# Performance work log

Hardware: AMD Instinct MI355X
Metric: run time of the kernel (lower is better)

Reference implementation:

```python
import jax, jax.numpy as jnp
import numpy as np

EMBED = 128
HEADS = 8
HEAD_DIM = EMBED // HEADS


def setup_inputs() -> dict:
    key = jax.random.key(0)
    ks = jax.random.split(key, 11)
    B, T, N, C = 8, 64, 170, EMBED
    s = 1.0 / np.sqrt(C)
    return {
        "values": jax.random.normal(ks[0], (B, T, N, C), dtype=jnp.float32),
        "keys": jax.random.normal(ks[1], (B, T, N, C), dtype=jnp.float32),
        "query": jax.random.normal(ks[2], (B, T, N, C), dtype=jnp.float32),
        "Wv": jax.random.normal(ks[3], (C, C), dtype=jnp.float32) * s,
        "bv": jnp.zeros((C,), dtype=jnp.float32),
        "Wk": jax.random.normal(ks[4], (C, C), dtype=jnp.float32) * s,
        "bk": jnp.zeros((C,), dtype=jnp.float32),
        "Wq": jax.random.normal(ks[5], (C, C), dtype=jnp.float32) * s,
        "bq": jnp.zeros((C,), dtype=jnp.float32),
        "Wo": jax.random.normal(ks[6], (C, C), dtype=jnp.float32) * s,
        "bo": jnp.zeros((C,), dtype=jnp.float32),
    }


def reference(values, keys, query, Wv, bv, Wk, bk, Wq, bq, Wo, bo):
    B, T, N, C = query.shape
    H, D = HEADS, HEAD_DIM
    # Linear projections (torch nn.Linear: x @ W.T + b)
    v = (values @ Wv.T + bv).reshape(B, T, N, H, D)
    k = (keys @ Wk.T + bk).reshape(B, T, N, H, D)
    q = (query @ Wq.T + bq).reshape(B, T, N, H, D)
    # spatial mode: attention over nodes N, independent per (b, t, h)
    energy = jnp.einsum('btqhd,btkhd->btqkh', q, k)  # [B,T,N,N,H]
    scale = jnp.asarray(C, q.dtype) ** 0.5
    attn = jax.nn.softmax(energy / scale, axis=3)
    out = jnp.einsum('btqkh,btkhd->btqhd', attn, v).reshape(B, T, N, H * D)
    return out @ Wo.T + bo
```

## Files before the change

kernel.cpp:

```cpp
#include <hip/hip_runtime.h>
#include <cstdint>

typedef float   f32x4  __attribute__((ext_vector_type(4)));
typedef __bf16  bf16x4 __attribute__((ext_vector_type(4)));
typedef __bf16  bf16x8 __attribute__((ext_vector_type(8)));

#if __has_builtin(__builtin_amdgcn_exp2f)
#define EXP2F(x) __builtin_amdgcn_exp2f(x)
#else
#define EXP2F(x) exp2f(x)
#endif

#define BT_TOTAL 512
#define NNODES 170
#define CDIM 128
#define HEADS 8
#define HDIM 16
#define SLAB (NNODES*HDIM)
#define NPAD 176
#define VSLAB (HDIM*NPAD)
#define QKV_ELEMS ((size_t)BT_TOTAL*HEADS*SLAB)
#define WPAD 136
#define S2L2E 0.12753851f

__global__ __launch_bounds__(256) void wconv_kernel(const float* __restrict__ wq,
                                                    const float* __restrict__ wk,
                                                    const float* __restrict__ wv,
                                                    const float* __restrict__ wo,
                                                    __bf16* __restrict__ wbf) {
    int idx = blockIdx.x * 256 + threadIdx.x;
    if (idx >= 4 * 16384) return;
    int mat = idx >> 14, rem = idx & 16383;
    int c = rem >> 7, o = rem & 127;
    int kk = o >> 5, l4 = (o & 31) >> 3, j = o & 7;
    int col = kk * 32 + l4 * 4 + (j & 3) + 16 * (j >> 2);
    const float* W = (mat == 0) ? wq : (mat == 1) ? wk : (mat == 2) ? wv : wo;
    float scale = (mat == 0) ? S2L2E : 1.0f;
    wbf[idx] = (__bf16)(W[c * 128 + col] * scale);
}

__global__ __launch_bounds__(256, 4) void qkv_kernel(const float* __restrict__ qin,
    const float* __restrict__ kin, const float* __restrict__ vin,
    const __bf16* __restrict__ wbf,
    const float* __restrict__ bq, const float* __restrict__ bk, const float* __restrict__ bv,
    __bf16* __restrict__ qws, __bf16* __restrict__ kws, __bf16* __restrict__ vt) {
    __shared__ __bf16 Wl[128 * WPAD];
    int t = threadIdx.x;
    int iid = blockIdx.x / BT_TOTAL;
    int bt  = blockIdx.x % BT_TOTAL;
    const float* X    = (iid == 0) ? qin : (iid == 1) ? kin : vin;
    const float* bias = (iid == 0) ? bq  : (iid == 1) ? bk  : bv;
    float wscale = (iid == 0) ? S2L2E : 1.0f;
    const __bf16* wb = wbf + iid * 16384;
    #pragma unroll
    for (int i = 0; i < 8; ++i) {
        int idx = i * 256 + t;
        int c = idx >> 4, x = (idx & 15) * 8;
        *(bf16x8*)&Wl[c * WPAD + x] = *(const bf16x8*)&wb[idx * 8];
    }
    __syncthreads();

    int w = t >> 6, lane = t & 63, li = lane & 15, l4 = lane >> 4;
    const f32x4 zf = {0.f, 0.f, 0.f, 0.f};

    auto loadA = [&](f32x4* A, int tile) {
        int mrow = tile * 16 + li;
        bool v = mrow < NNODES;
        const float* xr = X + ((size_t)(bt * NNODES + mrow)) * CDIM;
        #pragma unroll
        for (int kk = 0; kk < 4; ++kk) {
            A[2 * kk]     = v ? *(const f32x4*)(xr + kk * 32 + l4 * 4)      : zf;
            A[2 * kk + 1] = v ? *(const f32x4*)(xr + kk * 32 + l4 * 4 + 16) : zf;
        }
    };
    auto compute = [&](const f32x4* A, int tile) {
        f32x4 acc[8] = {};
        #pragma unroll
        for (int kk = 0; kk < 4; ++kk) {
            f32x4 a0 = A[2 * kk], a1 = A[2 * kk + 1];
            bf16x8 a = { (__bf16)a0[0], (__bf16)a0[1], (__bf16)a0[2], (__bf16)a0[3],
                         (__bf16)a1[0], (__bf16)a1[1], (__bf16)a1[2], (__bf16)a1[3] };
            #pragma unroll
            for (int nt = 0; nt < 8; ++nt) {
                bf16x8 b = *(const bf16x8*)&Wl[(nt * 16 + li) * WPAD + kk * 32 + l4 * 8];
                if (iid < 2)
                    acc[nt] = __builtin_amdgcn_mfma_f32_16x16x32_bf16(b, a, acc[nt], 0, 0, 0);
                else
                    acc[nt] = __builtin_amdgcn_mfma_f32_16x16x32_bf16(a, b, acc[nt], 0, 0, 0);
            }
        }
        if (iid < 2) {
            __bf16* dst = ((iid == 0) ? qws : kws) + (size_t)bt * HEADS * SLAB;
            int n = tile * 16 + li;
            if (n < NNODES) {
                #pragma unroll
                for (int nt = 0; nt < 8; ++nt) {
                    f32x4 b4 = *(const f32x4*)&bias[nt * 16 + l4 * 4];
                    f32x4 ov = acc[nt] + b4 * wscale;
                    bf16x4 o4 = { (__bf16)ov[0], (__bf16)ov[1], (__bf16)ov[2], (__bf16)ov[3] };
                    *(bf16x4*)&dst[(size_t)nt * SLAB + n * HDIM + l4 * 4] = o4;
                }
            }
        } else {
            __bf16* dst = vt + (size_t)bt * HEADS * VSLAB;
            int n0 = tile * 16 + l4 * 4;
            #pragma unroll
            for (int nt = 0; nt < 8; ++nt) {
                float bval = bias[nt * 16 + li];
                __bf16* d2 = dst + (size_t)nt * VSLAB + li * NPAD + n0;
                if (n0 + 3 < NNODES) {
                    bf16x4 o4 = { (__bf16)(acc[nt][0] + bval), (__bf16)(acc[nt][1] + bval),
                                  (__bf16)(acc[nt][2] + bval), (__bf16)(acc[nt][3] + bval) };
                    *(bf16x4*)d2 = o4;
                } else {
                    #pragma unroll
                    for (int r = 0; r < 4; ++r)
                        if (n0 + r < NNODES) d2[r] = (__bf16)(acc[nt][r] + bval);
                }
            }
        }
    };

    f32x4 A0[8], A1[8];
    loadA(A0, w);
    loadA(A1, w + 4);
    compute(A0, w);
    if (w < 3) loadA(A0, w + 8);
    compute(A1, w + 4);
    if (w < 3) compute(A0, w + 8);
}

__global__ __launch_bounds__(256) void attn_kernel(const __bf16* __restrict__ qws,
                                                   const __bf16* __restrict__ kws,
                                                   const __bf16* __restrict__ vt,
                                                   __bf16* __restrict__ ows) {
    int unit = blockIdx.x * 4 + (threadIdx.x >> 6);
    int half = unit & 1, bh = unit >> 1;
    int bt = bh >> 3, h = bh & 7;
    int lane = threadIdx.x & 63, li = lane & 15, l4 = lane >> 4;
    const __bf16* qb  = qws + ((size_t)(bt * HEADS + h)) * SLAB;
    const __bf16* kb  = kws + ((size_t)(bt * HEADS + h)) * SLAB;
    const __bf16* vtb = vt  + ((size_t)(bt * HEADS + h)) * VSLAB;
    __bf16* ob = ows + (size_t)bt * NNODES * CDIM + (h >> 1) * 32 + (h & 1) * 4;
    const __bf16 bz = (__bf16)0.0f;
    const bf16x4 z4 = {bz, bz, bz, bz};
    const f32x4 zf = {0.f, 0.f, 0.f, 0.f};

    bf16x4 kf[11];
    #pragma unroll
    for (int tt = 0; tt < 11; ++tt)
        kf[tt] = *(const bf16x4*)&kb[(tt * 16 + li) * HDIM + l4 * 4];

    bf16x8 vf[6];
    #pragma unroll
    for (int s = 0; s < 5; ++s) {
        bf16x4 a = *(const bf16x4*)&vtb[li * NPAD + 32 * s + 4 * l4];
        bf16x4 b = *(const bf16x4*)&vtb[li * NPAD + 32 * s + 4 * l4 + 16];
        vf[s] = __builtin_shufflevector(a, b, 0, 1, 2, 3, 4, 5, 6, 7);
    }
    {
        bf16x4 a = *(const bf16x4*)&vtb[li * NPAD + 160 + 4 * l4];
        bf16x8 v5 = { (160 + 4 * l4 + 0 < NNODES) ? a[0] : bz,
                      (160 + 4 * l4 + 1 < NNODES) ? a[1] : bz,
                      (160 + 4 * l4 + 2 < NNODES) ? a[2] : bz,
                      (160 + 4 * l4 + 3 < NNODES) ? a[3] : bz,
                      bz, bz, bz, bz };
        vf[5] = v5;
    }

    int q0 = half ? 6 : 0;
    int qn = half ? 5 : 6;
    for (int qi = 0; qi < qn; ++qi) {
        int qc = q0 + qi;
        bf16x4 qv = *(const bf16x4*)&qb[(qc * 16 + li) * HDIM + l4 * 4];
        bf16x8 qf = __builtin_shufflevector(qv, z4, 0, 1, 2, 3, 4, 5, 6, 7);
        bf16x4 ph[11];
        f32x4 s4 = zf;
        #pragma unroll
        for (int tt = 0; tt < 11; ++tt) {
            bf16x8 a = __builtin_shufflevector(kf[tt], z4, 0, 1, 2, 3, 4, 5, 6, 7);
            f32x4 e = __builtin_amdgcn_mfma_f32_16x16x32_bf16(a, qf, zf, 0, 0, 0);
            if (tt == 10) {
                #pragma unroll
                for (int r = 0; r < 4; ++r)
                    e[r] = (160 + l4 * 4 + r < NNODES) ? e[r] : -1.0e30f;
            }
            f32x4 p;
            p[0] = EXP2F(e[0]); p[1] = EXP2F(e[1]);
            p[2] = EXP2F(e[2]); p[3] = EXP2F(e[3]);
            s4 += p;
            ph[tt] = __builtin_convertvector(p, bf16x4);
        }
        float sum = (s4[0] + s4[1]) + (s4[2] + s4[3]);
        sum += __shfl_xor(sum, 16);
        sum += __shfl_xor(sum, 32);
        float inv = 1.0f / sum;
        f32x4 o0 = zf, o1 = zf;
        o0 = __builtin_amdgcn_mfma_f32_16x16x32_bf16(vf[0],
                __builtin_shufflevector(ph[0], ph[1], 0,1,2,3,4,5,6,7), o0, 0,0,0);
        o1 = __builtin_amdgcn_mfma_f32_16x16x32_bf16(vf[1],
                __builtin_shufflevector(ph[2], ph[3], 0,1,2,3,4,5,6,7), o1, 0,0,0);
        o0 = __builtin_amdgcn_mfma_f32_16x16x32_bf16(vf[2],
                __builtin_shufflevector(ph[4], ph[5], 0,1,2,3,4,5,6,7), o0, 0,0,0);
        o1 = __builtin_amdgcn_mfma_f32_16x16x32_bf16(vf[3],
                __builtin_shufflevector(ph[6], ph[7], 0,1,2,3,4,5,6,7), o1, 0,0,0);
        o0 = __builtin_amdgcn_mfma_f32_16x16x32_bf16(vf[4],
                __builtin_shufflevector(ph[8], ph[9], 0,1,2,3,4,5,6,7), o0, 0,0,0);
        o1 = __builtin_amdgcn_mfma_f32_16x16x32_bf16(vf[5],
                __builtin_shufflevector(ph[10], z4,    0,1,2,3,4,5,6,7), o1, 0,0,0);
        f32x4 o = (o0 + o1) * inv;
        int q = qc * 16 + li;
        if (q < NNODES) {
            bf16x4 ov = { (__bf16)o[0], (__bf16)o[1], (__bf16)o[2], (__bf16)o[3] };
            *(bf16x4*)&ob[(size_t)q * CDIM + l4 * 8] = ov;
        }
    }
}

__global__ __launch_bounds__(512) void oproj_kernel(const __bf16* __restrict__ ows,
                                                    const __bf16* __restrict__ wbf,
                                                    const float* __restrict__ bo,
                                                    float* __restrict__ out) {
    __shared__ __bf16 Wl[128 * WPAD];
    int t = threadIdx.x;
    int bt = blockIdx.x;
    const __bf16* wo = wbf + 3 * 16384;
    #pragma unroll
    for (int i = 0; i < 4; ++i) {
        int idx = i * 512 + t;
        int c = idx >> 4, x = (idx & 15) * 8;
        *(bf16x8*)&Wl[c * WPAD + x] = *(const bf16x8*)&wo[idx * 8];
    }
    __syncthreads();

    int w = t >> 6, lane = t & 63, li = lane & 15, l4 = lane >> 4;
    const bf16x8 z8 = {};

    auto loadO = [&](bf16x8* A, int tile) {
        int mrow = tile * 16 + li;
        bool v = mrow < NNODES;
        const __bf16* ar = ows + ((size_t)(bt * NNODES + mrow)) * CDIM;
        #pragma unroll
        for (int kk = 0; kk < 4; ++kk)
            A[kk] = v ? *(const bf16x8*)(ar + kk * 32 + l4 * 8) : z8;
    };
    auto computeO = [&](const bf16x8* A, int tile) {
        f32x4 acc[8] = {};
        #pragma unroll
        for (int kk = 0; kk < 4; ++kk) {
            #pragma unroll
            for (int nt = 0; nt < 8; ++nt) {
                bf16x8 b = *(const bf16x8*)&Wl[(nt * 16 + li) * WPAD + kk * 32 + l4 * 8];
                acc[nt] = __builtin_amdgcn_mfma_f32_16x16x32_bf16(b, A[kk], acc[nt], 0, 0, 0);
            }
        }
        int n = tile * 16 + li;
        if (n < NNODES) {
            float* orow = out + ((size_t)bt * NNODES + n) * CDIM;
            #pragma unroll
            for (int nt = 0; nt < 8; ++nt) {
                f32x4 b4 = *(const f32x4*)&bo[nt * 16 + l4 * 4];
                *(f32x4*)&orow[nt * 16 + l4 * 4] = acc[nt] + b4;
            }
        }
    };

    bf16x8 A0[4], A1[4];
    loadO(A0, w);
    if (w < 3) loadO(A1, w + 8);
    computeO(A0, w);
    if (w < 3) computeO(A1, w + 8);
}

extern "C" void kernel_launch(void* const* d_in, const int* in_sizes, int n_in,
                              void* d_out, int out_size, void* d_ws, size_t ws_size,
                              hipStream_t stream) {
    const float* values = (const float*)d_in[0];
    const float* keys   = (const float*)d_in[1];
    const float* query  = (const float*)d_in[2];
    const float* Wv = (const float*)d_in[3];
    const float* bv = (const float*)d_in[4];
    const float* Wk = (const float*)d_in[5];
    const float* bk = (const float*)d_in[6];
    const float* Wq = (const float*)d_in[7];
    const float* bq = (const float*)d_in[8];
    const float* Wo = (const float*)d_in[9];
    const float* bo = (const float*)d_in[10];
    float* out = (float*)d_out;

    __bf16* qws = (__bf16*)d_ws;
    __bf16* kws = qws + QKV_ELEMS;
    __bf16* ows = kws + QKV_ELEMS;
    __bf16* wbf = ows + QKV_ELEMS;
    __bf16* vt  = (__bf16*)d_out;

    hipLaunchKernelGGL(wconv_kernel, dim3(256),  dim3(256), 0, stream, Wq, Wk, Wv, Wo, wbf);
    hipLaunchKernelGGL(qkv_kernel,   dim3(1536), dim3(256), 0, stream,
                       query, keys, values, wbf, bq, bk, bv, qws, kws, vt);
    hipLaunchKernelGGL(attn_kernel,  dim3(2048), dim3(256), 0, stream, qws, kws, vt, ows);
    hipLaunchKernelGGL(oproj_kernel, dim3(512),  dim3(512), 0, stream, ows, wbf, bo, out);
}
```

Before: 103.5 us.

## Restructure QKV projection over flat rows with async global-to-LDS staging

The QKV projection kernel now tiles the flattened B*T*N row space in 64-row blocks instead of one (b,t) slab per block, which removes the padding waste of 170-node slabs. Input rows are staged into a double-buffered LDS tile using global_load_lds with a swizzled layout to avoid bank conflicts. Each wave keeps its half of the weight matrix in registers rather than in a shared LDS weight tile. The trade-offs are more blocks, per-row div/mod by 170 in the epilogue, and higher register pressure from holding weight fragments.

Result: slower. 113.5 us (+9.7%).

```diff
diff --git a/kernel.cpp b/kernel.cpp
--- a/kernel.cpp
+++ b/kernel.cpp
@@ -22,6 +22,13 @@
 #define QKV_ELEMS ((size_t)BT_TOTAL*HEADS*SLAB)
 #define WPAD 136
 #define S2L2E 0.12753851f
+#define MROWS (BT_TOTAL*NNODES)
+#define BLKS_PER_IID 1360
+
+__device__ __forceinline__ void gload_lds16(const float* g, float* l) {
+    __builtin_amdgcn_global_load_lds((const __attribute__((address_space(1))) uint32_t*)g,
+                                     (__attribute__((address_space(3))) uint32_t*)l, 16, 0, 0);
+}
 
 __global__ __launch_bounds__(256) void wconv_kernel(const float* __restrict__ wq,
                                                     const float* __restrict__ wk,
@@ -44,90 +51,102 @@
     const __bf16* __restrict__ wbf,
     const float* __restrict__ bq, const float* __restrict__ bk, const float* __restrict__ bv,
     __bf16* __restrict__ qws, __bf16* __restrict__ kws, __bf16* __restrict__ vt) {
-    __shared__ __bf16 Wl[128 * WPAD];
-    int t = threadIdx.x;
-    int iid = blockIdx.x / BT_TOTAL;
-    int bt  = blockIdx.x % BT_TOTAL;
+    __shared__ __align__(16) float Xl[2][32 * 128];
+
+    int bid = blockIdx.x;
+    int iid = bid / BLKS_PER_IID, blk = bid % BLKS_PER_IID;
     const float* X    = (iid == 0) ? qin : (iid == 1) ? kin : vin;
     const float* bias = (iid == 0) ? bq  : (iid == 1) ? bk  : bv;
     float wscale = (iid == 0) ? S2L2E : 1.0f;
+    int t = threadIdx.x, w = t >> 6, lane = t & 63, li = lane & 15, l4 = lane >> 4;
+    int gbase = blk * 64;
+    int ch = (w >> 1) * 64;
+    int wt = w & 1;
+
     const __bf16* wb = wbf + iid * 16384;
+    bf16x8 wf[4][4];
     #pragma unroll
-    for (int i = 0; i < 8; ++i) {
-        int idx = i * 256 + t;
-        int c = idx >> 4, x = (idx & 15) * 8;
-        *(bf16x8*)&Wl[c * WPAD + x] = *(const bf16x8*)&wb[idx * 8];
-    }
-    __syncthreads();
-
-    int w = t >> 6, lane = t & 63, li = lane & 15, l4 = lane >> 4;
-    const f32x4 zf = {0.f, 0.f, 0.f, 0.f};
-
-    auto loadA = [&](f32x4* A, int tile) {
-        int mrow = tile * 16 + li;
-        bool v = mrow < NNODES;
-        const float* xr = X + ((size_t)(bt * NNODES + mrow)) * CDIM;
+    for (int nt = 0; nt < 4; ++nt)
+        #pragma unroll
+        for (int kk = 0; kk < 4; ++kk)
+            wf[nt][kk] = *(const bf16x8*)&wb[(ch + nt * 16 + li) * 128 + kk * 32 + l4 * 8];
+
+    auto stage = [&](int buf, int tt) {
+        float* dst0 = &Xl[buf][w * 8 * 128];
+        int g0 = gbase + tt * 32 + w * 8;
+        int rloc = (lane >> 5);
+        int pc = lane & 31;
+        #pragma unroll
+        for (int i = 0; i < 4; ++i) {
+            int r = 2 * i + rloc;
+            int lc = (pc - 4 * (r & 7)) & 31;
+            const float* src = X + (size_t)(g0 + r) * 128 + lc * 4;
+            gload_lds16(src, dst0 + i * 256);
+        }
+    };
+
+    auto compute = [&](int buf, int tt) {
+        int r = wt * 16 + li;
+        f32x4 acc[4] = {};
         #pragma unroll
         for (int kk = 0; kk < 4; ++kk) {
-            A[2 * kk]     = v ? *(const f32x4*)(xr + kk * 32 + l4 * 4)      : zf;
-            A[2 * kk + 1] = v ? *(const f32x4*)(xr + kk * 32 + l4 * 4 + 16) : zf;
-        }
-    };
-    auto compute = [&](const f32x4* A, int tile) {
-        f32x4 acc[8] = {};
-        #pragma unroll
-        for (int kk = 0; kk < 4; ++kk) {
-            f32x4 a0 = A[2 * kk], a1 = A[2 * kk + 1];
+            int p1 = (8 * kk + l4 + 4 * (li & 7)) & 31;
+            int p2 = (8 * kk + l4 + 4 + 4 * (li & 7)) & 31;
+            f32x4 a0 = *(const f32x4*)&Xl[buf][r * 128 + p1 * 4];
+            f32x4 a1 = *(const f32x4*)&Xl[buf][r * 128 + p2 * 4];
             bf16x8 a = { (__bf16)a0[0], (__bf16)a0[1], (__bf16)a0[2], (__bf16)a0[3],
                          (__bf16)a1[0], (__bf16)a1[1], (__bf16)a1[2], (__bf16)a1[3] };
+            if (iid < 2) {
+                #pragma unroll
+                for (int nt = 0; nt < 4; ++nt)
+                    acc[nt] = __builtin_amdgcn_mfma_f32_16x16x32_bf16(wf[nt][kk], a, acc[nt], 0, 0, 0);
+            } else {
+                #pragma unroll
+                for (int nt = 0; nt < 4; ++nt)
+                    acc[nt] = __builtin_amdgcn_mfma_f32_16x16x32_bf16(a, wf[nt][kk], acc[nt], 0, 0, 0);
+            }
+        }
+        if (iid < 2) {
+            int g = gbase + tt * 32 + wt * 16 + li;
+            int bt = g / 170, n = g - bt * 170;
+            __bf16* base = ((iid == 0) ? qws : kws);
             #pragma unroll
-            for (int nt = 0; nt < 8; ++nt) {
-                bf16x8 b = *(const bf16x8*)&Wl[(nt * 16 + li) * WPAD + kk * 32 + l4 * 8];
-                if (iid < 2)
-                    acc[nt] = __builtin_amdgcn_mfma_f32_16x16x32_bf16(b, a, acc[nt], 0, 0, 0);
-                else
-                    acc[nt] = __builtin_amdgcn_mfma_f32_16x16x32_bf16(a, b, acc[nt], 0, 0, 0);
-            }
-        }
-        if (iid < 2) {
-            __bf16* dst = ((iid == 0) ? qws : kws) + (size_t)bt * HEADS * SLAB;
-            int n = tile * 16 + li;
-            if (n < NNODES) {
-                #pragma unroll
-                for (int nt = 0; nt < 8; ++nt) {
-                    f32x4 b4 = *(const f32x4*)&bias[nt * 16 + l4 * 4];
-                    f32x4 ov = acc[nt] + b4 * wscale;
-                    bf16x4 o4 = { (__bf16)ov[0], (__bf16)ov[1], (__bf16)ov[2], (__bf16)ov[3] };
-                    *(bf16x4*)&dst[(size_t)nt * SLAB + n * HDIM + l4 * 4] = o4;
-                }
+            for (int nt = 0; nt < 4; ++nt) {
+                int h = (w >> 1) * 4 + nt;
+                f32x4 b4 = *(const f32x4*)&bias[ch + nt * 16 + l4 * 4];
+                f32x4 ov = acc[nt] + b4 * wscale;
+                bf16x4 o4 = { (__bf16)ov[0], (__bf16)ov[1], (__bf16)ov[2], (__bf16)ov[3] };
+                *(bf16x4*)&base[((size_t)(bt * HEADS + h)) * SLAB + n * HDIM + l4 * 4] = o4;
             }
         } else {
-            __bf16* dst = vt + (size_t)bt * HEADS * VSLAB;
-            int n0 = tile * 16 + l4 * 4;
+            int n0g = gbase + tt * 32 + wt * 16 + 4 * l4;
+            int bt0 = n0g / 170, n0 = n0g - bt0 * 170;
             #pragma unroll
-            for (int nt = 0; nt < 8; ++nt) {
-                float bval = bias[nt * 16 + li];
-                __bf16* d2 = dst + (size_t)nt * VSLAB + li * NPAD + n0;
-                if (n0 + 3 < NNODES) {
+            for (int nt = 0; nt < 4; ++nt) {
+                int h = (w >> 1) * 4 + nt;
+                float bval = bias[ch + nt * 16 + li];
+                if (n0 <= 166) {
                     bf16x4 o4 = { (__bf16)(acc[nt][0] + bval), (__bf16)(acc[nt][1] + bval),
                                   (__bf16)(acc[nt][2] + bval), (__bf16)(acc[nt][3] + bval) };
-                    *(bf16x4*)d2 = o4;
+                    *(bf16x4*)&vt[((size_t)(bt0 * HEADS + h)) * VSLAB + li * NPAD + n0] = o4;
                 } else {
                     #pragma unroll
-                    for (int r = 0; r < 4; ++r)
-                        if (n0 + r < NNODES) d2[r] = (__bf16)(acc[nt][r] + bval);
+                    for (int rr = 0; rr < 4; ++rr) {
+                        int g = n0g + rr;
+                        int bt = g / 170, n = g - bt * 170;
+                        vt[((size_t)(bt * HEADS + h)) * VSLAB + li * NPAD + n] = (__bf16)(acc[nt][rr] + bval);
+                    }
                 }
             }
         }
     };
 
-    f32x4 A0[8], A1[8];
-    loadA(A0, w);
-    loadA(A1, w + 4);
-    compute(A0, w);
-    if (w < 3) loadA(A0, w + 8);
-    compute(A1, w + 4);
-    if (w < 3) compute(A0, w + 8);
+    stage(0, 0);
+    __syncthreads();
+    stage(1, 1);
+    compute(0, 0);
+    __syncthreads();
+    compute(1, 1);
 }
 
 __global__ __launch_bounds__(256) void attn_kernel(const __bf16* __restrict__ qws,
@@ -295,7 +314,7 @@
     __bf16* vt  = (__bf16*)d_out;
 
     hipLaunchKernelGGL(wconv_kernel, dim3(256),  dim3(256), 0, stream, Wq, Wk, Wv, Wo, wbf);
-    hipLaunchKernelGGL(qkv_kernel,   dim3(1536), dim3(256), 0, stream,
+    hipLaunchKernelGGL(qkv_kernel,   dim3(3 * BLKS_PER_IID), dim3(256), 0, stream,
                        query, keys, values, wbf, bq, bk, bv, qws, kws, vt);
     hipLaunchKernelGGL(attn_kernel,  dim3(2048), dim3(256), 0, stream, qws, kws, vt, ows);
     hipLaunchKernelGGL(oproj_kernel, dim3(512),  dim3(512), 0, stream, ows, wbf, bo, out);
```

## Fuse attention and output projection into one kernel via LDS staging

Applied to the files above, without the earlier changes.

Merges the attention and output-projection kernels: each block handles one (b,t) with one wave per head, writes the per-head attention output into shared memory, then runs the Wo projection from LDS. This removes the bf16 intermediate round trip through global memory and one kernel launch. V is moved from the output buffer into the workspace, and the final stores become nontemporal. In exchange, blocks use large LDS and there are fewer, longer waves per block, which reduces occupancy and parallelism.

Result: slower. 122.9 us (+18.8%).

```diff
diff --git a/kernel.cpp b/kernel.cpp
--- a/kernel.cpp
+++ b/kernel.cpp
@@ -20,7 +20,9 @@
 #define NPAD 176
 #define VSLAB (HDIM*NPAD)
 #define QKV_ELEMS ((size_t)BT_TOTAL*HEADS*SLAB)
+#define VT_ELEMS  ((size_t)BT_TOTAL*HEADS*VSLAB)
 #define WPAD 136
+#define OPAD 136
 #define S2L2E 0.12753851f
 
 __global__ __launch_bounds__(256) void wconv_kernel(const float* __restrict__ wq,
@@ -114,8 +116,8 @@
                     *(bf16x4*)d2 = o4;
                 } else {
                     #pragma unroll
-                    for (int r = 0; r < 4; ++r)
-                        if (n0 + r < NNODES) d2[r] = (__bf16)(acc[nt][r] + bval);
+                    for (int rr = 0; rr < 4; ++rr)
+                        if (n0 + rr < NNODES) d2[rr] = (__bf16)(acc[nt][rr] + bval);
                 }
             }
         }
@@ -130,128 +132,115 @@
     if (w < 3) compute(A0, w + 8);
 }
 
-__global__ __launch_bounds__(256) void attn_kernel(const __bf16* __restrict__ qws,
-                                                   const __bf16* __restrict__ kws,
-                                                   const __bf16* __restrict__ vt,
-                                                   __bf16* __restrict__ ows) {
-    int unit = blockIdx.x * 4 + (threadIdx.x >> 6);
-    int half = unit & 1, bh = unit >> 1;
-    int bt = bh >> 3, h = bh & 7;
-    int lane = threadIdx.x & 63, li = lane & 15, l4 = lane >> 4;
-    const __bf16* qb  = qws + ((size_t)(bt * HEADS + h)) * SLAB;
-    const __bf16* kb  = kws + ((size_t)(bt * HEADS + h)) * SLAB;
-    const __bf16* vtb = vt  + ((size_t)(bt * HEADS + h)) * VSLAB;
-    __bf16* ob = ows + (size_t)bt * NNODES * CDIM + (h >> 1) * 32 + (h & 1) * 4;
+__global__ __launch_bounds__(512, 4) void attn_oproj_kernel(const __bf16* __restrict__ qws,
+    const __bf16* __restrict__ kws, const __bf16* __restrict__ vt,
+    const __bf16* __restrict__ wbf, const float* __restrict__ bo,
+    float* __restrict__ out) {
+    __shared__ __align__(16) __bf16 Wl[128 * OPAD];
+    __shared__ __align__(16) __bf16 oL[NNODES * OPAD];
+
+    int bt = blockIdx.x;
+    int t = threadIdx.x, w = t >> 6, lane = t & 63, li = lane & 15, l4 = lane >> 4;
     const __bf16 bz = (__bf16)0.0f;
     const bf16x4 z4 = {bz, bz, bz, bz};
     const f32x4 zf = {0.f, 0.f, 0.f, 0.f};
 
-    bf16x4 kf[11];
-    #pragma unroll
-    for (int tt = 0; tt < 11; ++tt)
-        kf[tt] = *(const bf16x4*)&kb[(tt * 16 + li) * HDIM + l4 * 4];
-
-    bf16x8 vf[6];
-    #pragma unroll
-    for (int s = 0; s < 5; ++s) {
-        bf16x4 a = *(const bf16x4*)&vtb[li * NPAD + 32 * s + 4 * l4];
-        bf16x4 b = *(const bf16x4*)&vtb[li * NPAD + 32 * s + 4 * l4 + 16];
-        vf[s] = __builtin_shufflevector(a, b, 0, 1, 2, 3, 4, 5, 6, 7);
-    }
-    {
-        bf16x4 a = *(const bf16x4*)&vtb[li * NPAD + 160 + 4 * l4];
-        bf16x8 v5 = { (160 + 4 * l4 + 0 < NNODES) ? a[0] : bz,
-                      (160 + 4 * l4 + 1 < NNODES) ? a[1] : bz,
-                      (160 + 4 * l4 + 2 < NNODES) ? a[2] : bz,
-                      (160 + 4 * l4 + 3 < NNODES) ? a[3] : bz,
-                      bz, bz, bz, bz };
-        vf[5] = v5;
-    }
-
-    int q0 = half ? 6 : 0;
-    int qn = half ? 5 : 6;
-    for (int qi = 0; qi < qn; ++qi) {
-        int qc = q0 + qi;
-        bf16x4 qv = *(const bf16x4*)&qb[(qc * 16 + li) * HDIM + l4 * 4];
-        bf16x8 qf = __builtin_shufflevector(qv, z4, 0, 1, 2, 3, 4, 5, 6, 7);
-        bf16x4 ph[11];
-        f32x4 s4 = zf;
-        #pragma unroll
-        for (int tt = 0; tt < 11; ++tt) {
-            bf16x8 a = __builtin_shufflevector(kf[tt], z4, 0, 1, 2, 3, 4, 5, 6, 7);
-            f32x4 e = __builtin_amdgcn_mfma_f32_16x16x32_bf16(a, qf, zf, 0, 0, 0);
-            if (tt == 10) {
-                #pragma unroll
-                for (int r = 0; r < 4; ++r)
-                    e[r] = (160 + l4 * 4 + r < NNODES) ? e[r] : -1.0e30f;
-            }
-            f32x4 p;
-            p[0] = EXP2F(e[0]); p[1] = EXP2F(e[1]);
-            p[2] = EXP2F(e[2]); p[3] = EXP2F(e[3]);
-            s4 += p;
-            ph[tt] = __builtin_convertvector(p, bf16x4);
-        }
-        float sum = (s4[0] + s4[1]) + (s4[2] + s4[3]);
-        sum += __shfl_xor(sum, 16);
-        sum += __shfl_xor(sum, 32);
-        float inv = 1.0f / sum;
-        f32x4 o0 = zf, o1 = zf;
-        o0 = __builtin_amdgcn_mfma_f32_16x16x32_bf16(vf[0],
-                __builtin_shufflevector(ph[0], ph[1], 0,1,2,3,4,5,6,7), o0, 0,0,0);
-        o1 = __builtin_amdgcn_mfma_f32_16x16x32_bf16(vf[1],
-                __builtin_shufflevector(ph[2], ph[3], 0,1,2,3,4,5,6,7), o1, 0,0,0);
-        o0 = __builtin_amdgcn_mfma_f32_16x16x32_bf16(vf[2],
-                __builtin_shufflevector(ph[4], ph[5], 0,1,2,3,4,5,6,7), o0, 0,0,0);
-        o1 = __builtin_amdgcn_mfma_f32_16x16x32_bf16(vf[3],
-                __builtin_shufflevector(ph[6], ph[7], 0,1,2,3,4,5,6,7), o1, 0,0,0);
-        o0 = __builtin_amdgcn_mfma_f32_16x16x32_bf16(vf[4],
-                __builtin_shufflevector(ph[8], ph[9], 0,1,2,3,4,5,6,7), o0, 0,0,0);
-        o1 = __builtin_amdgcn_mfma_f32_16x16x32_bf16(vf[5],
-                __builtin_shufflevector(ph[10], z4,    0,1,2,3,4,5,6,7), o1, 0,0,0);
-        f32x4 o = (o0 + o1) * inv;
-        int q = qc * 16 + li;
-        if (q < NNODES) {
-            bf16x4 ov = { (__bf16)o[0], (__bf16)o[1], (__bf16)o[2], (__bf16)o[3] };
-            *(bf16x4*)&ob[(size_t)q * CDIM + l4 * 8] = ov;
-        }
-    }
-}
-
-__global__ __launch_bounds__(512) void oproj_kernel(const __bf16* __restrict__ ows,
-                                                    const __bf16* __restrict__ wbf,
-                                                    const float* __restrict__ bo,
-                                                    float* __restrict__ out) {
-    __shared__ __bf16 Wl[128 * WPAD];
-    int t = threadIdx.x;
-    int bt = blockIdx.x;
     const __bf16* wo = wbf + 3 * 16384;
     #pragma unroll
     for (int i = 0; i < 4; ++i) {
         int idx = i * 512 + t;
         int c = idx >> 4, x = (idx & 15) * 8;
-        *(bf16x8*)&Wl[c * WPAD + x] = *(const bf16x8*)&wo[idx * 8];
+        *(bf16x8*)&Wl[c * OPAD + x] = *(const bf16x8*)&wo[idx * 8];
+    }
+
+    {
+        int h = w;
+        const __bf16* qb  = qws + ((size_t)(bt * HEADS + h)) * SLAB;
+        const __bf16* kb  = kws + ((size_t)(bt * HEADS + h)) * SLAB;
+        const __bf16* vtb = vt  + ((size_t)(bt * HEADS + h)) * VSLAB;
+
+        bf16x4 kf[11];
+        #pragma unroll
+        for (int tt = 0; tt < 11; ++tt)
+            kf[tt] = *(const bf16x4*)&kb[(tt * 16 + li) * HDIM + l4 * 4];
+
+        bf16x8 vf[6];
+        #pragma unroll
+        for (int s = 0; s < 5; ++s) {
+            bf16x4 a = *(const bf16x4*)&vtb[li * NPAD + 32 * s + 4 * l4];
+            bf16x4 b = *(const bf16x4*)&vtb[li * NPAD + 32 * s + 4 * l4 + 16];
+            vf[s] = __builtin_shufflevector(a, b, 0, 1, 2, 3, 4, 5, 6, 7);
+        }
+        {
+            bf16x4 a = *(const bf16x4*)&vtb[li * NPAD + 160 + 4 * l4];
+            bf16x8 v5 = { (160 + 4 * l4 + 0 < NNODES) ? a[0] : bz,
+                          (160 + 4 * l4 + 1 < NNODES) ? a[1] : bz,
+                          (160 + 4 * l4 + 2 < NNODES) ? a[2] : bz,
+                          (160 + 4 * l4 + 3 < NNODES) ? a[3] : bz,
+                          bz, bz, bz, bz };
+            vf[5] = v5;
+        }
+
+        int ocol = (h >> 1) * 32 + (h & 1) * 4 + l4 * 8;
+        #pragma unroll 1
+        for (int qc = 0; qc < 11; ++qc) {
+            bf16x4 qv = *(const bf16x4*)&qb[(qc * 16 + li) * HDIM + l4 * 4];
+            bf16x8 qf = __builtin_shufflevector(qv, z4, 0, 1, 2, 3, 4, 5, 6, 7);
+            bf16x4 ph[11];
+            f32x4 s4 = zf;
+            #pragma unroll
+            for (int tt = 0; tt < 11; ++tt) {
+                bf16x8 a = __builtin_shufflevector(kf[tt], z4, 0, 1, 2, 3, 4, 5, 6, 7);
+                f32x4 e = __builtin_amdgcn_mfma_f32_16x16x32_bf16(a, qf, zf, 0, 0, 0);
+                if (tt == 10) {
+                    #pragma unroll
+                    for (int r = 0; r < 4; ++r)
+                        e[r] = (160 + l4 * 4 + r < NNODES) ? e[r] : -1.0e30f;
+                }
+                f32x4 p;
+                p[0] = EXP2F(e[0]); p[1] = EXP2F(e[1]);
+                p[2] = EXP2F(e[2]); p[3] = EXP2F(e[3]);
+                s4 += p;
+                ph[tt] = __builtin_convertvector(p, bf16x4);
+            }
+            float sum = (s4[0] + s4[1]) + (s4[2] + s4[3]);
+            sum += __shfl_xor(sum, 16);
+            sum += __shfl_xor(sum, 32);
+            float inv = 1.0f / sum;
+            f32x4 o0 = zf, o1 = zf;
+            o0 = __builtin_amdgcn_mfma_f32_16x16x32_bf16(vf[0],
+                    __builtin_shufflevector(ph[0], ph[1], 0,1,2,3,4,5,6,7), o0, 0,0,0);
+            o1 = __builtin_amdgcn_mfma_f32_16x16x32_bf16(vf[1],
+                    __builtin_shufflevector(ph[2], ph[3], 0,1,2,3,4,5,6,7), o1, 0,0,0);
+            o0 = __builtin_amdgcn_mfma_f32_16x16x32_bf16(vf[2],
+                    __builtin_shufflevector(ph[4], ph[5], 0,1,2,3,4,5,6,7), o0, 0,0,0);
+            o1 = __builtin_amdgcn_mfma_f32_16x16x32_bf16(vf[3],
+                    __builtin_shufflevector(ph[6], ph[7], 0,1,2,3,4,5,6,7), o1, 0,0,0);
+            o0 = __builtin_amdgcn_mfma_f32_16x16x32_bf16(vf[4],
+                    __builtin_shufflevector(ph[8], ph[9], 0,1,2,3,4,5,6,7), o0, 0,0,0);
+            o1 = __builtin_amdgcn_mfma_f32_16x16x32_bf16(vf[5],
+                    __builtin_shufflevector(ph[10], z4,    0,1,2,3,4,5,6,7), o1, 0,0,0);
+            f32x4 o = (o0 + o1) * inv;
+            int q = qc * 16 + li;
+            if (q < NNODES) {
+                bf16x4 ov = { (__bf16)o[0], (__bf16)o[1], (__bf16)o[2], (__bf16)o[3] };
+                *(bf16x4*)&oL[(size_t)q * OPAD + ocol] = ov;
+            }
+        }
     }
     __syncthreads();
 
-    int w = t >> 6, lane = t & 63, li = lane & 15, l4 = lane >> 4;
-    const bf16x8 z8 = {};
-
-    auto loadO = [&](bf16x8* A, int tile) {
-        int mrow = tile * 16 + li;
-        bool v = mrow < NNODES;
-        const __bf16* ar = ows + ((size_t)(bt * NNODES + mrow)) * CDIM;
-        #pragma unroll
-        for (int kk = 0; kk < 4; ++kk)
-            A[kk] = v ? *(const bf16x8*)(ar + kk * 32 + l4 * 8) : z8;
-    };
-    auto computeO = [&](const bf16x8* A, int tile) {
+    for (int tile = w; tile < 11; tile += 8) {
+        int mr = tile * 16 + li;
+        if (mr > NNODES - 1) mr = NNODES - 1;
         f32x4 acc[8] = {};
         #pragma unroll
         for (int kk = 0; kk < 4; ++kk) {
-            #pragma unroll
-            for (int nt = 0; nt < 8; ++nt) {
-                bf16x8 b = *(const bf16x8*)&Wl[(nt * 16 + li) * WPAD + kk * 32 + l4 * 8];
-                acc[nt] = __builtin_amdgcn_mfma_f32_16x16x32_bf16(b, A[kk], acc[nt], 0, 0, 0);
+            bf16x8 a = *(const bf16x8*)&oL[(size_t)mr * OPAD + kk * 32 + l4 * 8];
+            #pragma unroll
+            for (int nt = 0; nt < 8; ++nt) {
+                bf16x8 b = *(const bf16x8*)&Wl[(nt * 16 + li) * OPAD + kk * 32 + l4 * 8];
+                acc[nt] = __builtin_amdgcn_mfma_f32_16x16x32_bf16(b, a, acc[nt], 0, 0, 0);
             }
         }
         int n = tile * 16 + li;
@@ -260,16 +249,11 @@
             #pragma unroll
             for (int nt = 0; nt < 8; ++nt) {
                 f32x4 b4 = *(const f32x4*)&bo[nt * 16 + l4 * 4];
-                *(f32x4*)&orow[nt * 16 + l4 * 4] = acc[nt] + b4;
-            }
-        }
-    };
-
-    bf16x8 A0[4], A1[4];
-    loadO(A0, w);
-    if (w < 3) loadO(A1, w + 8);
-    computeO(A0, w);
-    if (w < 3) computeO(A1, w + 8);
+                f32x4 ov = acc[nt] + b4;
+                __builtin_nontemporal_store(ov, (f32x4*)&orow[nt * 16 + l4 * 4]);
+            }
+        }
+    }
 }
 
 extern "C" void kernel_launch(void* const* d_in, const int* in_sizes, int n_in,
@@ -290,13 +274,12 @@
 
     __bf16* qws = (__bf16*)d_ws;
     __bf16* kws = qws + QKV_ELEMS;
-    __bf16* ows = kws + QKV_ELEMS;
-    __bf16* wbf = ows + QKV_ELEMS;
-    __bf16* vt  = (__bf16*)d_out;
+    __bf16* vt  = kws + QKV_ELEMS;
+    __bf16* wbf = vt + VT_ELEMS;
 
     hipLaunchKernelGGL(wconv_kernel, dim3(256),  dim3(256), 0, stream, Wq, Wk, Wv, Wo, wbf);
     hipLaunchKernelGGL(qkv_kernel,   dim3(1536), dim3(256), 0, stream,
                        query, keys, values, wbf, bq, bk, bv, qws, kws, vt);
-    hipLaunchKernelGGL(attn_kernel,  dim3(2048), dim3(256), 0, stream, qws, kws, vt, ows);
-    hipLaunchKernelGGL(oproj_kernel, dim3(512),  dim3(512), 0, stream, ows, wbf, bo, out);
-}
+    hipLaunchKernelGGL(attn_oproj_kernel, dim3(BT_TOTAL), dim3(512), 0, stream,
+                       qws, kws, vt, wbf, bo, out);
+}
```
